# Performance work log

Hardware: AMD Instinct MI355X
Metric: run time of the kernel (lower is better)

The kernel has to match this reference:

```python
import jax, jax.numpy as jnp
import numpy as np

B, K, D, H, ZDIM = 65536, 16, 64, 128, 16

def setup_inputs() -> dict:
    key = jax.random.key(0)
    ks = jax.random.split(key, 20)
    s = 0.05
    inp = {
        'z': jax.random.normal(ks[0], (B, ZDIM), dtype=jnp.float32),
        'y': jax.random.randint(ks[1], (B,), 0, K),
        # backbone: 4 fc blocks (Linear+ReLU)
        'bw0': jax.random.normal(ks[2], (ZDIM, H), dtype=jnp.float32) * s,
        'bb0': jnp.zeros((H,), dtype=jnp.float32),
        'bw1': jax.random.normal(ks[3], (H, H), dtype=jnp.float32) * s,
        'bb1': jnp.zeros((H,), dtype=jnp.float32),
        'bw2': jax.random.normal(ks[4], (H, H), dtype=jnp.float32) * s,
        'bb2': jnp.zeros((H,), dtype=jnp.float32),
        'bw3': jax.random.normal(ks[5], (H, H), dtype=jnp.float32) * s,
        'bb3': jnp.zeros((H,), dtype=jnp.float32),
        # K heads, weights stacked on leading expert axis; layers 0-2 have ReLU, layer 3 does not
        'hw0': jax.random.normal(ks[6], (K, H, H), dtype=jnp.float32) * s,
        'hb0': jnp.zeros((K, H), dtype=jnp.float32),
        'hw1': jax.random.normal(ks[7], (K, H, H), dtype=jnp.float32) * s,
        'hb1': jnp.zeros((K, H), dtype=jnp.float32),
        'hw2': jax.random.normal(ks[8], (K, H, H), dtype=jnp.float32) * s,
        'hb2': jnp.zeros((K, H), dtype=jnp.float32),
        'hw3': jax.random.normal(ks[9], (K, H, D), dtype=jnp.float32) * s,
        'hb3': jnp.zeros((K, D), dtype=jnp.float32),
    }
    return inp

def reference(z, y, bw0, bb0, bw1, bb1, bw2, bb2, bw3, bb3,
              hw0, hb0, hw1, hb1, hw2, hb2, hw3, hb3):
    h = jax.nn.relu(z @ bw0 + bb0)
    h = jax.nn.relu(h @ bw1 + bb1)
    h = jax.nn.relu(h @ bw2 + bb2)
    h = jax.nn.relu(h @ bw3 + bb3)          # [B, H]
    # all K expert heads (faithful to original: compute all, then gather)
    a = jax.nn.relu(jnp.einsum('bi,kij->bkj', h, hw0) + hb0)  # [B, K, H]
    a = jax.nn.relu(jnp.einsum('bki,kij->bkj', a, hw1) + hb1)
    a = jax.nn.relu(jnp.einsum('bki,kij->bkj', a, hw2) + hb2)
    a = jnp.einsum('bki,kij->bkj', a, hw3) + hb3              # [B, K, D], no ReLU
    # select the y-th head per sample
    out = jnp.take_along_axis(a, y[:, None, None], axis=1)[:, 0, :]  # [B, D]
    return out
```

## Files before the change

kernel.cpp:

```cpp
#include <hip/hip_runtime.h>
#include <hip/hip_bf16.h>
#include <stdint.h>


typedef _Float16 f16;
typedef __attribute__((ext_vector_type(2)))  _Float16 f16x2;
typedef __attribute__((ext_vector_type(4)))  _Float16 f16x4;
typedef __attribute__((ext_vector_type(8)))  _Float16 f16x8;
typedef __attribute__((ext_vector_type(16))) float    f32x16;
typedef uint32_t u32;
typedef __attribute__((ext_vector_type(2))) u32 u32x2;
typedef __attribute__((ext_vector_type(4))) u32 u32x4;

#define MFMA(a, b, c) __builtin_amdgcn_mfma_f32_32x32x16_f16((a), (b), (c), 0, 0, 0)

constexpr int Bc = 65536;
constexpr int Kc = 16;
constexpr int Hc = 128;
constexpr int Dc = 64;

constexpr int CAP  = 4608;
constexpr int SPB  = 128;
constexpr int BPE  = CAP / SPB;
constexpr int NBLK = Kc * BPE;
constexpr int NXCD = 8;
constexpr int CHUNK = NBLK / NXCD;

constexpr float INV_LOSCALE = 1.0f / 1024.0f;

constexpr int BBW_F16 = 2048 + 3 * 16384;
constexpr int HWE_F16 = 3 * 16384 + 8192;

constexpr int PREP_BLKS = 52 + Kc * 56;

struct Act { f16x8 w[8]; };

__device__ __forceinline__ f32x16 zero16() {
    f32x16 z;
#pragma unroll
    for (int i = 0; i < 16; ++i) z[i] = 0.0f;
    return z;
}

__device__ __forceinline__ void gload16(const f16* g, f16* l) {
    __builtin_amdgcn_global_load_lds(
        (const __attribute__((address_space(1))) void*)g,
        (__attribute__((address_space(3))) void*)l, 16, 0, 0);
}

__device__ __forceinline__ void stage_q(f16* dst, const f16* gHi, const f16* gLo,
                                        int wid, int lane) {
#pragma unroll
    for (int i = 0; i < 2; ++i) {
        const int seg = wid * 2 + i;
        gload16(gHi + seg * 512 + lane * 8, dst + seg * 512);
        gload16(gLo + seg * 512 + lane * 8, dst + 4096 + seg * 512);
    }
}

template<bool RELU>
__device__ __forceinline__ void build_windows(
    const f32x16& c0, const f32x16& c1, const float4* bq,
    f16x8& w0, f16x8& w1)
{
    u32 P[8];
#pragma unroll
    for (int g = 0; g < 4; ++g) {
        const float bb[4] = {bq[g].x, bq[g].y, bq[g].z, bq[g].w};
        f16 h[4];
#pragma unroll
        for (int j = 0; j < 4; ++j) {
            float v = fmaf(c0[4 * g + j] + c1[4 * g + j], INV_LOSCALE, bb[j]);
            if (RELU) v = fmaxf(v, 0.0f);
            h[j] = (f16)v;
        }
        f16x2 p0; p0[0] = h[0]; p0[1] = h[1];
        f16x2 p1; p1[0] = h[2]; p1[1] = h[3];
        P[2 * g]     = __builtin_bit_cast(u32, p0);
        P[2 * g + 1] = __builtin_bit_cast(u32, p1);
    }
    const u32x2 r02 = __builtin_amdgcn_permlane32_swap(P[0], P[2], false, false);
    const u32x2 r13 = __builtin_amdgcn_permlane32_swap(P[1], P[3], false, false);
    const u32x2 r46 = __builtin_amdgcn_permlane32_swap(P[4], P[6], false, false);
    const u32x2 r57 = __builtin_amdgcn_permlane32_swap(P[5], P[7], false, false);
    u32x4 W0 = { r02[0], r13[0], r02[1], r13[1] };
    u32x4 W1 = { r46[0], r57[0], r46[1], r57[1] };
    w0 = __builtin_bit_cast(f16x8, W0);
    w1 = __builtin_bit_cast(f16x8, W1);
}

template<bool STAGE_NEXT>
__device__ __forceinline__ void layer_lds(
    f16* lds, int& par, const Act& src, Act& dst,
    const f16* gHi, const f16* gLo, const f16* gHiN, const f16* gLoN,
    const float* __restrict__ biasG, int wid, int lane, int bh)
{
#pragma unroll
    for (int q = 0; q < 4; ++q) {
        if (q < 3)
            stage_q(lds + (par ^ 1) * 8192, gHi + (q + 1) * 4096,
                    gLo + (q + 1) * 4096, wid, lane);
        else if (STAGE_NEXT)
            stage_q(lds + (par ^ 1) * 8192, gHiN, gLoN, wid, lane);

        float4 bq[4];
#pragma unroll
        for (int g = 0; g < 4; ++g)
            bq[g] = *(const float4*)(biasG + 32 * q + 8 * g + 4 * bh);

        const f16* pw = lds + par * 8192 + lane * 8;
        f32x16 c0 = zero16(), c1 = zero16();
        __builtin_amdgcn_s_setprio(1);
#pragma unroll
        for (int ks = 0; ks < 8; ++ks) {
            const f16x8 wh = *(const f16x8*)(pw + ks * 512);
            const f16x8 wl = *(const f16x8*)(pw + 4096 + ks * 512);
            c0 = MFMA(wh, src.w[ks], c0);
            c1 = MFMA(wl, src.w[ks], c1);
        }
        __builtin_amdgcn_s_setprio(0);
        build_windows<true>(c0, c1, bq, dst.w[2 * q], dst.w[2 * q + 1]);
        __syncthreads();
        par ^= 1;
    }
}

__device__ __forceinline__ void layer_final(
    f16* lds, int& par, const Act& src,
    const f16* gHi, const f16* gLo, const float* __restrict__ biasG,
    float* __restrict__ out, int bidx, int wid, int lane, int bh)
{
#pragma unroll
    for (int q = 0; q < 2; ++q) {
        if (q == 0)
            stage_q(lds + (par ^ 1) * 8192, gHi + 4096, gLo + 4096, wid, lane);

        float4 bq[4];
#pragma unroll
        for (int g = 0; g < 4; ++g)
            bq[g] = *(const float4*)(biasG + 32 * q + 8 * g + 4 * bh);

        const f16* pw = lds + par * 8192 + lane * 8;
        f32x16 c0 = zero16(), c1 = zero16();
        __builtin_amdgcn_s_setprio(1);
#pragma unroll
        for (int ks = 0; ks < 8; ++ks) {
            const f16x8 wh = *(const f16x8*)(pw + ks * 512);
            const f16x8 wl = *(const f16x8*)(pw + 4096 + ks * 512);
            c0 = MFMA(wh, src.w[ks], c0);
            c1 = MFMA(wl, src.w[ks], c1);
        }
        __builtin_amdgcn_s_setprio(0);
        if (bidx >= 0) {
#pragma unroll
            for (int g = 0; g < 4; ++g) {
                float4 v;
                v.x = fmaf(c0[4 * g + 0] + c1[4 * g + 0], INV_LOSCALE, bq[g].x);
                v.y = fmaf(c0[4 * g + 1] + c1[4 * g + 1], INV_LOSCALE, bq[g].y);
                v.z = fmaf(c0[4 * g + 2] + c1[4 * g + 2], INV_LOSCALE, bq[g].z);
                v.w = fmaf(c0[4 * g + 3] + c1[4 * g + 3], INV_LOSCALE, bq[g].w);
                *(float4*)(out + (size_t)bidx * Dc + 32 * q + 8 * g + 4 * bh) = v;
            }
        }
        if (q == 0) __syncthreads();
        par ^= 1;
    }
}

__global__ __launch_bounds__(256, 3) void fused_mlp(
    const float* __restrict__ z,
    const int* __restrict__ idxb, const int* __restrict__ cursor,
    const f16* __restrict__ bbH, const f16* __restrict__ bbL,
    const float* __restrict__ bb0, const float* __restrict__ bb1,
    const float* __restrict__ bb2, const float* __restrict__ bb3,
    const f16* __restrict__ hH, const f16* __restrict__ hL,
    const float* __restrict__ hb0, const float* __restrict__ hb1,
    const float* __restrict__ hb2, const float* __restrict__ hb3,
    float* __restrict__ out)
{
    __shared__ __attribute__((aligned(16))) f16 WLDS[2 * 8192];

    const int blk = (blockIdx.x % NXCD) * CHUNK + blockIdx.x / NXCD;
    const int e = blk / BPE;
    const int local0 = (blk % BPE) * SPB;
    const int cnt = min(cursor[e * 16], CAP);
    if (cnt - local0 <= 0) return;

    const int tid = threadIdx.x;
    const int wid = tid >> 6, lane = tid & 63;
    const int l31 = lane & 31, bh = lane >> 5;

    int bidx = -1;
    const int sIdx = local0 + wid * 32 + l31;
    if (sIdx < cnt) bidx = idxb[e * CAP + sIdx];

    f16x8 zw;
    if (bidx >= 0) {
        const float4 u0 = *(const float4*)(z + (size_t)bidx * 16 + bh * 8);
        const float4 u1 = *(const float4*)(z + (size_t)bidx * 16 + bh * 8 + 4);
        zw[0] = (f16)u0.x; zw[1] = (f16)u0.y; zw[2] = (f16)u0.z; zw[3] = (f16)u0.w;
        zw[4] = (f16)u1.x; zw[5] = (f16)u1.y; zw[6] = (f16)u1.z; zw[7] = (f16)u1.w;
    } else {
#pragma unroll
        for (int j = 0; j < 8; ++j) zw[j] = (f16)0.0f;
    }

    stage_q(WLDS, bbH + 2048, bbL + 2048, wid, lane);

    Act aA, aB;
#pragma unroll
    for (int q = 0; q < 4; ++q) {
        float4 bq[4];
#pragma unroll
        for (int g = 0; g < 4; ++g)
            bq[g] = *(const float4*)(bb0 + 32 * q + 8 * g + 4 * bh);
        const f16x8 wh = *(const f16x8*)(bbH + q * 512 + lane * 8);
        const f16x8 wl = *(const f16x8*)(bbL + q * 512 + lane * 8);
        f32x16 c0 = zero16(), c1 = zero16();
        c0 = MFMA(wh, zw, c0);
        c1 = MFMA(wl, zw, c1);
        build_windows<true>(c0, c1, bq, aA.w[2 * q], aA.w[2 * q + 1]);
    }
    __syncthreads();
    int par = 0;

    layer_lds<true>(WLDS, par, aA, aB, bbH + 2048,  bbL + 2048,
                    bbH + 18432, bbL + 18432, bb1, wid, lane, bh);
    layer_lds<true>(WLDS, par, aB, aA, bbH + 18432, bbL + 18432,
                    bbH + 34816, bbL + 34816, bb2, wid, lane, bh);
    const size_t we = (size_t)e * HWE_F16;
    layer_lds<true>(WLDS, par, aA, aB, bbH + 34816, bbL + 34816,
                    hH + we, hL + we, bb3, wid, lane, bh);
    layer_lds<true>(WLDS, par, aB, aA, hH + we,         hL + we,
                    hH + we + 16384, hL + we + 16384, hb0 + e * Hc, wid, lane, bh);
    layer_lds<true>(WLDS, par, aA, aB, hH + we + 16384, hL + we + 16384,
                    hH + we + 32768, hL + we + 32768, hb1 + e * Hc, wid, lane, bh);
    layer_lds<true>(WLDS, par, aB, aA, hH + we + 32768, hL + we + 32768,
                    hH + we + 49152, hL + we + 49152, hb2 + e * Hc, wid, lane, bh);
    layer_final(WLDS, par, aA, hH + we + 49152, hL + we + 49152,
                hb3 + e * Dc, out, bidx, wid, lane, bh);
}

__global__ void prep_scatter(
    const float* __restrict__ bw0, const float* __restrict__ bw1,
    const float* __restrict__ bw2, const float* __restrict__ bw3,
    const float* __restrict__ hw0, const float* __restrict__ hw1,
    const float* __restrict__ hw2, const float* __restrict__ hw3,
    f16* __restrict__ bbH, f16* __restrict__ bbL,
    f16* __restrict__ hH,  f16* __restrict__ hL,
    const int* __restrict__ y, int* __restrict__ idxb, int* __restrict__ cursor)
{
    __shared__ float T[32][33];
    __shared__ int lc[Kc];
    __shared__ int lbase[Kc];
    const int id = blockIdx.x;
    const int tx = threadIdx.x;

    if (id >= PREP_BLKS) {
        if (tx < Kc) lc[tx] = 0;
        __syncthreads();
        const int b = (id - PREP_BLKS) * 256 + tx;
        const int e = y[b];
        const int r = atomicAdd(&lc[e], 1);
        __syncthreads();
        if (tx < Kc) lbase[tx] = atomicAdd(&cursor[tx * 16], lc[tx]);
        __syncthreads();
        const int slot = lbase[e] + r;
        if (slot < CAP) idxb[e * CAP + slot] = b;
        return;
    }

    const float* src; f16 *dh, *dl;
    int K, N, k0, n0;
    bool big;

    if (id < 52) {
        if (id < 4) {
            src = bw0; dh = bbH; dl = bbL;
            K = 16; N = 128; k0 = 0; n0 = id * 32; big = false;
        } else {
            const int t = id - 4;
            const int l = t / 16, tile = t % 16;
            const float* bws[3] = {bw1, bw2, bw3};
            src = bws[l];
            dh = bbH + 2048 + l * 16384;
            dl = bbL + 2048 + l * 16384;
            K = 128; N = 128; big = true;
            k0 = (tile >> 2) * 32; n0 = (tile & 3) * 32;
        }
    } else {
        const int t = id - 52;
        const int e = t / 56, r = t % 56;
        if (r < 48) {
            const int l = r / 16, tile = r % 16;
            const float* hws[3] = {hw0, hw1, hw2};
            src = hws[l] + (size_t)e * 16384;
            dh = hH + (size_t)e * HWE_F16 + l * 16384;
            dl = hL + (size_t)e * HWE_F16 + l * 16384;
            K = 128; N = 128; big = true;
            k0 = (tile >> 2) * 32; n0 = (tile & 3) * 32;
        } else {
            const int r2 = r - 48;
            src = hw3 + (size_t)e * 8192;
            dh = hH + (size_t)e * HWE_F16 + 49152;
            dl = hL + (size_t)e * HWE_F16 + 49152;
            K = 128; N = 64; big = true;
            k0 = (r2 >> 1) * 32; n0 = (r2 & 1) * 32;
        }
    }

    const int c = tx & 31, g = tx >> 5;
#pragma unroll
    for (int i = 0; i < 4; ++i) {
        const int row = g * 4 + i;
        if (k0 + row < K)
            T[c][row] = src[(size_t)(k0 + row) * N + n0 + c];
    }
    __syncthreads();
#pragma unroll
    for (int i = 0; i < 4; ++i) {
        const int n = n0 + g * 4 + i;
        const int k = k0 + c;
        if (k < K) {
            const float v = T[g * 4 + i][c];
            const float hif = (float)(f16)v;
            const f16 hi = (f16)(hif * 1024.0f);
            const f16 lo = (f16)((v - hif) * 1024.0f);
            size_t didx;
            if (big)
                didx = (size_t)(n >> 5) * 4096 + (size_t)(k >> 4) * 512
                     + ((k >> 3) & 1) * 256 + (n & 31) * 8 + (k & 7);
            else
                didx = (size_t)(n >> 5) * 512 + (size_t)(k >> 3) * 256
                     + (n & 31) * 8 + (k & 7);
            dh[didx] = hi;
            dl[didx] = lo;
        }
    }
}

extern "C" void kernel_launch(void* const* d_in, const int* in_sizes, int n_in,
                              void* d_out, int out_size, void* d_ws, size_t ws_size,
                              hipStream_t stream)
{
    const float* z   = (const float*)d_in[0];
    const int*   y   = (const int*)d_in[1];
    const float* bw0 = (const float*)d_in[2];
    const float* bb0 = (const float*)d_in[3];
    const float* bw1 = (const float*)d_in[4];
    const float* bb1 = (const float*)d_in[5];
    const float* bw2 = (const float*)d_in[6];
    const float* bb2 = (const float*)d_in[7];
    const float* bw3 = (const float*)d_in[8];
    const float* bb3 = (const float*)d_in[9];
    const float* hw0 = (const float*)d_in[10];
    const float* hb0 = (const float*)d_in[11];
    const float* hw1 = (const float*)d_in[12];
    const float* hb1 = (const float*)d_in[13];
    const float* hw2 = (const float*)d_in[14];
    const float* hb2 = (const float*)d_in[15];
    const float* hw3 = (const float*)d_in[16];
    const float* hb3 = (const float*)d_in[17];
    float* out = (float*)d_out;

    char* p = (char*)d_ws;
    f16* bbH = (f16*)p;  p += (size_t)BBW_F16 * 2;
    f16* bbL = (f16*)p;  p += (size_t)BBW_F16 * 2;
    f16* hH  = (f16*)p;  p += (size_t)Kc * HWE_F16 * 2;
    f16* hL  = (f16*)p;  p += (size_t)Kc * HWE_F16 * 2;
    int* idxb = (int*)p; p += (size_t)Kc * CAP * 4;
    int* cursor = (int*)p;

    hipMemsetAsync(cursor, 0, 256 * sizeof(int), stream);

    prep_scatter<<<PREP_BLKS + Bc / 256, 256, 0, stream>>>(
        bw0, bw1, bw2, bw3, hw0, hw1, hw2, hw3,
        bbH, bbL, hH, hL, y, idxb, cursor);

    fused_mlp<<<NBLK, 256, 0, stream>>>(
        z, idxb, cursor, bbH, bbL, bb0, bb1, bb2, bb3,
        hH, hL, hb0, hb1, hb2, hb3, out);
}
```

Baseline: 142.3 us.

## Replace double-buffered weight staging with triple-buffer ring and partial vmcnt waits

Weight-chunk staging moves from a two-slot LDS buffer with a full __syncthreads per chunk to a three-slot ring that prefetches two chunks ahead. Each phase waits only on older loads via a partial vmcnt wait plus barrier. All biases are also preloaded into LDS once per block instead of read from global memory in every phase. This aims to hide global-to-LDS latency behind MFMA work, at the cost of more LDS per block (which may limit occupancy at 3 blocks/CU) and a correctness dependence on the exact vmcnt count.

```diff
diff --git a/kernel.cpp b/kernel.cpp
--- a/kernel.cpp
+++ b/kernel.cpp
@@ -58,6 +58,12 @@
     }
 }
 
+__device__ __forceinline__ void phase_sync() {
+    asm volatile("s_waitcnt vmcnt(4)" ::: "memory");
+    __builtin_amdgcn_s_barrier();
+    __builtin_amdgcn_sched_barrier(0);
+}
+
 template<bool RELU>
 __device__ __forceinline__ void build_windows(
     const f32x16& c0, const f32x16& c1, const float4* bq,
@@ -89,26 +95,34 @@
     w1 = __builtin_bit_cast(f16x8, W1);
 }
 
-template<bool STAGE_NEXT>
-__device__ __forceinline__ void layer_lds(
-    f16* lds, int& par, const Act& src, Act& dst,
-    const f16* gHi, const f16* gLo, const f16* gHiN, const f16* gLoN,
-    const float* __restrict__ biasG, int wid, int lane, int bh)
+template<int I>
+__device__ __forceinline__ void layer_ring(
+    f16* ring, const Act& src, Act& dst,
+    const f16* gHi, const f16* gLo,
+    const f16* gHiN, const f16* gLoN,
+    const float* biasLds, int wid, int lane, int bh)
 {
 #pragma unroll
     for (int q = 0; q < 4; ++q) {
-        if (q < 3)
-            stage_q(lds + (par ^ 1) * 8192, gHi + (q + 1) * 4096,
-                    gLo + (q + 1) * 4096, wid, lane);
-        else if (STAGE_NEXT)
-            stage_q(lds + (par ^ 1) * 8192, gHiN, gLoN, wid, lane);
+        const int p = 4 * I + q;
+        const int cslot = p % 3;
+        const int sslot = (p + 2) % 3;
+
+        phase_sync();
+
+        if (q < 2)
+            stage_q(ring + sslot * 8192, gHi + (q + 2) * 4096,
+                    gLo + (q + 2) * 4096, wid, lane);
+        else
+            stage_q(ring + sslot * 8192, gHiN + (q - 2) * 4096,
+                    gLoN + (q - 2) * 4096, wid, lane);
 
         float4 bq[4];
 #pragma unroll
         for (int g = 0; g < 4; ++g)
-            bq[g] = *(const float4*)(biasG + 32 * q + 8 * g + 4 * bh);
-
-        const f16* pw = lds + par * 8192 + lane * 8;
+            bq[g] = *(const float4*)(biasLds + 32 * q + 8 * g + 4 * bh);
+
+        const f16* pw = ring + cslot * 8192 + lane * 8;
         f32x16 c0 = zero16(), c1 = zero16();
         __builtin_amdgcn_s_setprio(1);
 #pragma unroll
@@ -120,50 +134,6 @@
         }
         __builtin_amdgcn_s_setprio(0);
         build_windows<true>(c0, c1, bq, dst.w[2 * q], dst.w[2 * q + 1]);
-        __syncthreads();
-        par ^= 1;
-    }
-}
-
-__device__ __forceinline__ void layer_final(
-    f16* lds, int& par, const Act& src,
-    const f16* gHi, const f16* gLo, const float* __restrict__ biasG,
-    float* __restrict__ out, int bidx, int wid, int lane, int bh)
-{
-#pragma unroll
-    for (int q = 0; q < 2; ++q) {
-        if (q == 0)
-            stage_q(lds + (par ^ 1) * 8192, gHi + 4096, gLo + 4096, wid, lane);
-
-        float4 bq[4];
-#pragma unroll
-        for (int g = 0; g < 4; ++g)
-            bq[g] = *(const float4*)(biasG + 32 * q + 8 * g + 4 * bh);
-
-        const f16* pw = lds + par * 8192 + lane * 8;
-        f32x16 c0 = zero16(), c1 = zero16();
-        __builtin_amdgcn_s_setprio(1);
-#pragma unroll
-        for (int ks = 0; ks < 8; ++ks) {
-            const f16x8 wh = *(const f16x8*)(pw + ks * 512);
-            const f16x8 wl = *(const f16x8*)(pw + 4096 + ks * 512);
-            c0 = MFMA(wh, src.w[ks], c0);
-            c1 = MFMA(wl, src.w[ks], c1);
-        }
-        __builtin_amdgcn_s_setprio(0);
-        if (bidx >= 0) {
-#pragma unroll
-            for (int g = 0; g < 4; ++g) {
-                float4 v;
-                v.x = fmaf(c0[4 * g + 0] + c1[4 * g + 0], INV_LOSCALE, bq[g].x);
-                v.y = fmaf(c0[4 * g + 1] + c1[4 * g + 1], INV_LOSCALE, bq[g].y);
-                v.z = fmaf(c0[4 * g + 2] + c1[4 * g + 2], INV_LOSCALE, bq[g].z);
-                v.w = fmaf(c0[4 * g + 3] + c1[4 * g + 3], INV_LOSCALE, bq[g].w);
-                *(float4*)(out + (size_t)bidx * Dc + 32 * q + 8 * g + 4 * bh) = v;
-            }
-        }
-        if (q == 0) __syncthreads();
-        par ^= 1;
     }
 }
 
@@ -178,7 +148,8 @@
     const float* __restrict__ hb2, const float* __restrict__ hb3,
     float* __restrict__ out)
 {
-    __shared__ __attribute__((aligned(16))) f16 WLDS[2 * 8192];
+    __shared__ __attribute__((aligned(16))) f16 RING[3 * 8192];
+    __shared__ __attribute__((aligned(16))) float BIASL[960];
 
     const int blk = (blockIdx.x % NXCD) * CHUNK + blockIdx.x / NXCD;
     const int e = blk / BPE;
@@ -189,6 +160,23 @@
     const int tid = threadIdx.x;
     const int wid = tid >> 6, lane = tid & 63;
     const int l31 = lane & 31, bh = lane >> 5;
+
+#pragma unroll
+    for (int r = 0; r < 4; ++r) {
+        const int i = r * 256 + tid;
+        if (i < 960) {
+            float v;
+            if      (i < 128) v = bb0[i];
+            else if (i < 256) v = bb1[i - 128];
+            else if (i < 384) v = bb2[i - 256];
+            else if (i < 512) v = bb3[i - 384];
+            else if (i < 640) v = hb0[e * Hc + i - 512];
+            else if (i < 768) v = hb1[e * Hc + i - 640];
+            else if (i < 896) v = hb2[e * Hc + i - 768];
+            else              v = hb3[e * Dc + i - 896];
+            BIASL[i] = v;
+        }
+    }
 
     int bidx = -1;
     const int sIdx = local0 + wid * 32 + l31;
@@ -205,15 +193,17 @@
         for (int j = 0; j < 8; ++j) zw[j] = (f16)0.0f;
     }
 
-    stage_q(WLDS, bbH + 2048, bbL + 2048, wid, lane);
+    stage_q(RING,        bbH + 2048,        bbL + 2048,        wid, lane);
+    stage_q(RING + 8192, bbH + 2048 + 4096, bbL + 2048 + 4096, wid, lane);
 
     Act aA, aB;
+    __syncthreads();
 #pragma unroll
     for (int q = 0; q < 4; ++q) {
         float4 bq[4];
 #pragma unroll
         for (int g = 0; g < 4; ++g)
-            bq[g] = *(const float4*)(bb0 + 32 * q + 8 * g + 4 * bh);
+            bq[g] = *(const float4*)(BIASL + 32 * q + 8 * g + 4 * bh);
         const f16x8 wh = *(const f16x8*)(bbH + q * 512 + lane * 8);
         const f16x8 wl = *(const f16x8*)(bbL + q * 512 + lane * 8);
         f32x16 c0 = zero16(), c1 = zero16();
@@ -221,24 +211,52 @@
         c1 = MFMA(wl, zw, c1);
         build_windows<true>(c0, c1, bq, aA.w[2 * q], aA.w[2 * q + 1]);
     }
+
+    const size_t we = (size_t)e * HWE_F16;
+    layer_ring<0>(RING, aA, aB, bbH + 2048,        bbL + 2048,
+                  bbH + 18432,       bbL + 18432,       BIASL + 128, wid, lane, bh);
+    layer_ring<1>(RING, aB, aA, bbH + 18432,       bbL + 18432,
+                  bbH + 34816,       bbL + 34816,       BIASL + 256, wid, lane, bh);
+    layer_ring<2>(RING, aA, aB, bbH + 34816,       bbL + 34816,
+                  hH + we,           hL + we,           BIASL + 384, wid, lane, bh);
+    layer_ring<3>(RING, aB, aA, hH + we,           hL + we,
+                  hH + we + 16384,   hL + we + 16384,   BIASL + 512, wid, lane, bh);
+    layer_ring<4>(RING, aA, aB, hH + we + 16384,   hL + we + 16384,
+                  hH + we + 32768,   hL + we + 32768,   BIASL + 640, wid, lane, bh);
+    layer_ring<5>(RING, aB, aA, hH + we + 32768,   hL + we + 32768,
+                  hH + we + 49152,   hL + we + 49152,   BIASL + 768, wid, lane, bh);
+
     __syncthreads();
-    int par = 0;
-
-    layer_lds<true>(WLDS, par, aA, aB, bbH + 2048,  bbL + 2048,
-                    bbH + 18432, bbL + 18432, bb1, wid, lane, bh);
-    layer_lds<true>(WLDS, par, aB, aA, bbH + 18432, bbL + 18432,
-                    bbH + 34816, bbL + 34816, bb2, wid, lane, bh);
-    const size_t we = (size_t)e * HWE_F16;
-    layer_lds<true>(WLDS, par, aA, aB, bbH + 34816, bbL + 34816,
-                    hH + we, hL + we, bb3, wid, lane, bh);
-    layer_lds<true>(WLDS, par, aB, aA, hH + we,         hL + we,
-                    hH + we + 16384, hL + we + 16384, hb0 + e * Hc, wid, lane, bh);
-    layer_lds<true>(WLDS, par, aA, aB, hH + we + 16384, hL + we + 16384,
-                    hH + we + 32768, hL + we + 32768, hb1 + e * Hc, wid, lane, bh);
-    layer_lds<true>(WLDS, par, aB, aA, hH + we + 32768, hL + we + 32768,
-                    hH + we + 49152, hL + we + 49152, hb2 + e * Hc, wid, lane, bh);
-    layer_final(WLDS, par, aA, hH + we + 49152, hL + we + 49152,
-                hb3 + e * Dc, out, bidx, wid, lane, bh);
+#pragma unroll
+    for (int q = 0; q < 2; ++q) {
+        float4 bq[4];
+#pragma unroll
+        for (int g = 0; g < 4; ++g)
+            bq[g] = *(const float4*)(BIASL + 896 + 32 * q + 8 * g + 4 * bh);
+
+        const f16* pw = RING + q * 8192 + lane * 8;
+        f32x16 c0 = zero16(), c1 = zero16();
+        __builtin_amdgcn_s_setprio(1);
+#pragma unroll
+        for (int ks = 0; ks < 8; ++ks) {
+            const f16x8 wh = *(const f16x8*)(pw + ks * 512);
+            const f16x8 wl = *(const f16x8*)(pw + 4096 + ks * 512);
+            c0 = MFMA(wh, aA.w[ks], c0);
+            c1 = MFMA(wl, aA.w[ks], c1);
+        }
+        __builtin_amdgcn_s_setprio(0);
+        if (bidx >= 0) {
+#pragma unroll
+            for (int g = 0; g < 4; ++g) {
+                float4 v;
+                v.x = fmaf(c0[4 * g + 0] + c1[4 * g + 0], INV_LOSCALE, bq[g].x);
+                v.y = fmaf(c0[4 * g + 1] + c1[4 * g + 1], INV_LOSCALE, bq[g].y);
+                v.z = fmaf(c0[4 * g + 2] + c1[4 * g + 2], INV_LOSCALE, bq[g].z);
+                v.w = fmaf(c0[4 * g + 3] + c1[4 * g + 3], INV_LOSCALE, bq[g].w);
+                *(float4*)(out + (size_t)bidx * Dc + 32 * q + 8 * g + 4 * bh) = v;
+            }
+        }
+    }
 }
 
 __global__ void prep_scatter(
```

Result: faster. 138.9 us (-2.4%).
